# Performance work log

Measured on AMD Instinct MI355X. Metric: run time of the kernel, lower is better.

Reference implementation:

```python
import jax, jax.numpy as jnp
import numpy as np

N, E, D, ED = 50000, 800000, 64, 2


def setup_inputs() -> dict:
    key = jax.random.key(0)
    ks = jax.random.split(key, 16)
    inp = {
        "h": jax.random.normal(ks[0], (N, D), jnp.float32),
        "coord": jax.random.normal(ks[1], (N, 3), jnp.float32),
        "edge_index": jax.random.randint(ks[2], (2, E), 0, N, jnp.int32),
        "edge_attr": jax.random.normal(ks[3], (E, ED), jnp.float32),
        # edge_mlp: Linear(2D+1+ED -> D), Linear(D -> D)
        "W_e1": jax.random.normal(ks[4], (2 * D + 1 + ED, D), jnp.float32) * 0.08,
        "b_e1": jnp.zeros((D,), jnp.float32),
        "W_e2": jax.random.normal(ks[5], (D, D), jnp.float32) * 0.12,
        "b_e2": jnp.zeros((D,), jnp.float32),
        # node_mlp: Linear(D+D -> D), Linear(D -> D)
        "W_n1": jax.random.normal(ks[6], (2 * D, D), jnp.float32) * 0.08,
        "b_n1": jnp.zeros((D,), jnp.float32),
        "W_n2": jax.random.normal(ks[7], (D, D), jnp.float32) * 0.12,
        "b_n2": jnp.zeros((D,), jnp.float32),
        # coord_mlp: Linear(D -> D), Linear(D -> 1, bias=False, xavier gain 0.001)
        "W_c1": jax.random.normal(ks[8], (D, D), jnp.float32) * 0.12,
        "b_c1": jnp.zeros((D,), jnp.float32),
        "W_c2": jax.random.normal(ks[9], (D, 1), jnp.float32) * 1e-3,
    }
    return inp


def reference(h, coord, edge_index, edge_attr,
              W_e1, b_e1, W_e2, b_e2,
              W_n1, b_n1, W_n2, b_n2,
              W_c1, b_c1, W_c2):
    row, col = edge_index[0], edge_index[1]
    n_nodes = h.shape[0]

    # coord2radial
    coord_diff = coord[row] - coord[col]                       # [E,3]
    radial = jnp.sum(coord_diff * coord_diff, axis=-1, keepdims=True)  # [E,1]

    # edge_model
    e_in = jnp.concatenate([h[row], h[col], radial, edge_attr], axis=-1)  # [E, 2D+1+ED]
    e = jax.nn.silu(e_in @ W_e1 + b_e1)
    edge_feat = jax.nn.silu(e @ W_e2 + b_e2)                   # [E,D]

    # coord_model: trans = coord_diff * coord_mlp(edge_feat), clamp, segment mean
    scale = jax.nn.silu(edge_feat @ W_c1 + b_c1) @ W_c2        # [E,1]
    trans = jnp.clip(coord_diff * scale, -100.0, 100.0)        # [E,3]
    agg_c = jax.ops.segment_sum(trans, row, num_segments=n_nodes)       # [N,3]
    cnt = jax.ops.segment_sum(jnp.ones((trans.shape[0],), trans.dtype), row,
                              num_segments=n_nodes)            # [N]
    coord_out = coord + agg_c / jnp.clip(cnt, 1.0, None)[:, None]  # coords_weight=1.0

    # node_model: segment sum of edge_feat by row, node MLP, residual
    agg_h = jax.ops.segment_sum(edge_feat, row, num_segments=n_nodes)   # [N,D]
    n_in = jnp.concatenate([h, agg_h], axis=-1)                # [N,2D]
    h_out = h + (jax.nn.silu(n_in @ W_n1 + b_n1) @ W_n2 + b_n2)

    return (h_out, coord_out)
```

## Files before the change

kernel.cpp:

```cpp
#include <hip/hip_runtime.h>

#define DD 64
#define SLOTMAX 64

using s8v   = __attribute__((ext_vector_type(8))) short;
using f32x4 = __attribute__((ext_vector_type(4))) float;

typedef unsigned int   uint_t;
typedef unsigned short ushort_t;

union U8 { s8v v; uint_t u[4]; };

__device__ __forceinline__ float silu_f(float x) {
    return x / (1.0f + __expf(-x));
}
__device__ __forceinline__ float clamp100(float x) {
    return fminf(fmaxf(x, -100.0f), 100.0f);
}
__device__ __forceinline__ unsigned short f2bf(float x) {
    unsigned int u = __float_as_uint(x);
    return (unsigned short)((u + 0x7FFFu + ((u >> 16) & 1u)) >> 16);
}
__device__ __forceinline__ float bf2f(ushort_t v) {
    return __uint_as_float(((uint_t)v) << 16);
}
__device__ __forceinline__ uint_t cvt_pk_bf16(float lo, float hi) {
    uint_t r;
    asm("v_cvt_pk_bf16_f32 %0, %1, %2" : "=v"(r) : "v"(lo), "v"(hi));
    return r;
}

#define WAVE_FENCE() do { asm volatile("s_waitcnt lgkmcnt(0)" ::: "memory"); \
                          __builtin_amdgcn_sched_barrier(0); } while (0)

__global__ __launch_bounds__(256) void prep_all(
    const float* __restrict__ h,
    const float* __restrict__ coord,
    const float* __restrict__ We1, const float* __restrict__ We2,
    const float* __restrict__ Wc1,
    const float* __restrict__ Wn1, const float* __restrict__ Wn2,
    const float* __restrict__ be1, const float* __restrict__ be2,
    const float* __restrict__ bc1,
    const int*   __restrict__ ei,
    ushort_t* __restrict__ hbf,
    ushort_t* __restrict__ wf,
    float4* __restrict__ coord4,
    int* __restrict__ cnt_i,
    int N, int E, int total8, int histBlocks, int hbfBlocks, int c4Blocks)
{
    const int b = blockIdx.x;
    if (b < histBlocks) {
        const int e = b * 256 + threadIdx.x;
        if (e < E) atomicAdd(&cnt_i[ei[e]], 1);
    } else if (b < histBlocks + hbfBlocks) {
        const int t = (b - histBlocks) * 256 + threadIdx.x;
        if (t < total8) {
            const float4 v0 = ((const float4*)h)[t * 2 + 0];
            const float4 v1 = ((const float4*)h)[t * 2 + 1];
            uint4 o;
            o.x = (uint_t)f2bf(v0.x) | ((uint_t)f2bf(v0.y) << 16);
            o.y = (uint_t)f2bf(v0.z) | ((uint_t)f2bf(v0.w) << 16);
            o.z = (uint_t)f2bf(v1.x) | ((uint_t)f2bf(v1.y) << 16);
            o.w = (uint_t)f2bf(v1.z) | ((uint_t)f2bf(v1.w) << 16);
            ((uint4*)hbf)[t] = o;
        }
    } else if (b < histBlocks + hbfBlocks + c4Blocks) {
        const int t = (b - histBlocks - hbfBlocks) * 256 + threadIdx.x;
        if (t < N) {
            float4 c;
            c.x = coord[3 * t + 0];
            c.y = coord[3 * t + 1];
            c.z = coord[3 * t + 2];
            c.w = 0.0f;
            coord4[t] = c;
        }
    } else {
        const int t = (b - histBlocks - hbfBlocks - c4Blocks) * 256 + threadIdx.x;
        if (t >= 32768) return;
        if (t < 28672) {
            const int j    = t & 7;
            const int lane = (t >> 3) & 63;
            const int n0   = (t >> 9) & 3;
            const int k0   = (t >> 11) & 1;
            const int mat  = t >> 12;
            const int g    = lane >> 4;
            int k;
            if (mat == 2 || mat == 3) k = 16 * (2 * k0 + (j >> 2)) + 4 * g + (j & 3);
            else                      k = k0 * 32 + g * 8 + j;
            const int n = n0 * 16 + (lane & 15);
            float v;
            if      (mat == 0) v = We1[(size_t)k * 64 + n];
            else if (mat == 1) v = We1[(size_t)(64 + k) * 64 + n];
            else if (mat == 2) v = We2[(size_t)k * 64 + n];
            else if (mat == 3) v = Wc1[(size_t)k * 64 + n];
            else if (mat == 4) v = Wn1[(size_t)k * 64 + n];
            else if (mat == 5) v = Wn1[(size_t)(64 + k) * 64 + n];
            else               v = Wn2[(size_t)k * 64 + n];
            wf[t] = f2bf(v);
        } else {
            const int t2   = t - 28672;
            const int j    = t2 & 7;
            const int lane = (t2 >> 3) & 63;
            const int n0   = (t2 >> 9) & 3;
            const int xm   = (t2 >> 11) & 1;
            const int k = 8 * (lane >> 4) + j;
            const int m = n0 * 16 + (lane & 15);
            float v = 0.0f;
            if (xm == 0) {
                if      (k == 0) v = We1[(size_t)128 * 64 + m];
                else if (k == 1) v = We1[(size_t)129 * 64 + m];
                else if (k == 2) v = We1[(size_t)130 * 64 + m];
                else if (k == 3) v = be1[m];
            } else {
                if      (k == 0) v = be2[m];
                else if (k == 1) v = bc1[m];
            }
            wf[t] = f2bf(v);
        }
    }
}

__global__ __launch_bounds__(256) void prep_scan(
    const int* __restrict__ cnt_i,
    int* __restrict__ cursor,
    int* __restrict__ nstart,
    int N)
{
    __shared__ int sdata[256];
    __shared__ int sbase;
    const int tid = threadIdx.x;
    const int n = blockIdx.x * 256 + tid;
    int deg = 0;
    if (n < N) { deg = cnt_i[n]; if (deg > SLOTMAX) deg = SLOTMAX; }
    sdata[tid] = deg;
    __syncthreads();
    for (int off = 1; off < 256; off <<= 1) {
        const int t = (tid >= off) ? sdata[tid - off] : 0;
        __syncthreads();
        sdata[tid] += t;
        __syncthreads();
    }
    if (tid == 255) sbase = atomicAdd(cursor, sdata[255]);
    __syncthreads();
    if (n < N) nstart[n] = sbase + sdata[tid] - deg;
}

__global__ __launch_bounds__(256) void prep_fill(
    const int* __restrict__ ei,
    const float* __restrict__ ea,
    const int* __restrict__ nstart,
    int* __restrict__ cnt2,
    int4* __restrict__ eperm4,
    int E)
{
    const int e = blockIdx.x * 256 + threadIdx.x;
    if (e >= E) return;
    const int r = ei[e];
    const int s = atomicAdd(&cnt2[r], 1);
    if (s < SLOTMAX) {
        const int c = ei[E + e];
        const float2 a2 = *(const float2*)(ea + 2 * (size_t)e);
        const uint_t pk = cvt_pk_bf16(a2.x, a2.y);
        int4 v; v.x = r; v.y = c; v.z = (int)pk; v.w = 0;
        eperm4[(size_t)nstart[r] + s] = v;
    }
}

__global__ __launch_bounds__(512, 4) void egcl_edge(
    const ushort_t* __restrict__ hbf,
    const ushort_t* __restrict__ wfG,
    const float4* __restrict__ coord4,
    const int4* __restrict__ eperm4,
    const int* __restrict__ cursorP,
    const float* __restrict__ Wc2,
    uint_t* __restrict__ efu,
    float4* __restrict__ trans4,
    int totalWaves)
{
    __shared__ ushort_t fragLDS[20480];

    const int tid = threadIdx.x;
    #pragma unroll
    for (int i = 0; i < 4; ++i)
        ((uint4*)fragLDS)[tid + i * 512] = ((const uint4*)wfG)[tid + i * 512];
    ((uint4*)fragLDS)[2048 + tid] = ((const uint4*)wfG)[3584 + tid];
    __syncthreads();

    const int P = cursorP[0];
    const int wid  = tid >> 6;
    const int lane = tid & 63;
    const int l15  = lane & 15;
    const int g    = lane >> 4;

#define LD_W(mat, k0, m0) \
    (*(const s8v*)(fragLDS + ((((mat)*2 + (k0))*4 + (m0)) * 512) + lane * 8))
#define LD_X7(m0) (*(const s8v*)(fragLDS + 16384 + (m0) * 512 + lane * 8))
#define LD_XB(m0) (*(const s8v*)(fragLDS + 18432 + (m0) * 512 + lane * 8))

    float wc2_c[4][4];
    #pragma unroll
    for (int m0 = 0; m0 < 4; ++m0)
        #pragma unroll
        for (int j = 0; j < 4; ++j)
            wc2_c[m0][j] = Wc2[m0 * 16 + 4 * g + j];

    U8 b2f, bcf;
    b2f.u[0] = 0x00003F80u; b2f.u[1] = 0; b2f.u[2] = 0; b2f.u[3] = 0;
    bcf.u[0] = 0x3F800000u; bcf.u[1] = 0; bcf.u[2] = 0; bcf.u[3] = 0;

    const f32x4 zero4 = {0.f, 0.f, 0.f, 0.f};

    for (int t = blockIdx.x * 8 + wid; t * 16 < P; t += totalWaves) {
        const int p   = t * 16 + l15;
        const bool val = (p < P);
        const int pL  = val ? p : (P - 1);

        const int4 e4 = eperm4[pL];
        const int row = e4.x;
        const int col = e4.y;
        const uint_t eap = (uint_t)e4.z;

        const float4 cr = coord4[row];
        const float4 cc = coord4[col];
        const ushort_t* hr = hbf + (size_t)row * 64;
        const ushort_t* hc = hbf + (size_t)col * 64;
        const s8v br0 = *(const s8v*)(hr + g * 8);
        const s8v br1 = *(const s8v*)(hr + 32 + g * 8);
        const s8v bc0 = *(const s8v*)(hc + g * 8);
        const s8v bc1 = *(const s8v*)(hc + 32 + g * 8);

        const float dx = cr.x - cc.x, dy = cr.y - cc.y, dz = cr.z - cc.z;
        const float radial = dx * dx + dy * dy + dz * dz;

        U8 ex;
        const float ea0f = __uint_as_float(eap << 16);
        ex.u[0] = cvt_pk_bf16(radial, ea0f);
        ex.u[1] = (eap >> 16) | 0x3F800000u;
        ex.u[2] = 0; ex.u[3] = 0;

        f32x4 c1[4];
        #pragma unroll
        for (int m0 = 0; m0 < 4; ++m0) {
            f32x4 a = zero4;
            a = __builtin_amdgcn_mfma_f32_16x16x32_bf16(LD_W(0, 0, m0), br0, a, 0, 0, 0);
            a = __builtin_amdgcn_mfma_f32_16x16x32_bf16(LD_W(0, 1, m0), br1, a, 0, 0, 0);
            a = __builtin_amdgcn_mfma_f32_16x16x32_bf16(LD_W(1, 0, m0), bc0, a, 0, 0, 0);
            a = __builtin_amdgcn_mfma_f32_16x16x32_bf16(LD_W(1, 1, m0), bc1, a, 0, 0, 0);
            a = __builtin_amdgcn_mfma_f32_16x16x32_bf16(LD_X7(m0),      ex.v, a, 0, 0, 0);
            c1[m0] = a;
        }

        U8 f2a, f2b;
        #pragma unroll
        for (int m0 = 0; m0 < 4; ++m0) {
            const float ya = silu_f(c1[m0][0]);
            const float yb = silu_f(c1[m0][1]);
            const float yc = silu_f(c1[m0][2]);
            const float yd = silu_f(c1[m0][3]);
            U8& dst = (m0 < 2) ? f2a : f2b;
            dst.u[(m0 & 1) * 2 + 0] = cvt_pk_bf16(ya, yb);
            dst.u[(m0 & 1) * 2 + 1] = cvt_pk_bf16(yc, yd);
        }

        f32x4 c2[4];
        #pragma unroll
        for (int m0 = 0; m0 < 4; ++m0) {
            f32x4 a = zero4;
            a = __builtin_amdgcn_mfma_f32_16x16x32_bf16(LD_W(2, 0, m0), f2a.v, a, 0, 0, 0);
            a = __builtin_amdgcn_mfma_f32_16x16x32_bf16(LD_W(2, 1, m0), f2b.v, a, 0, 0, 0);
            a = __builtin_amdgcn_mfma_f32_16x16x32_bf16(LD_XB(m0),      b2f.v, a, 0, 0, 0);
            c2[m0] = a;
        }

        uint_t* efrow = efu + (size_t)pL * 32;
        U8 f3a, f3b;
        #pragma unroll
        for (int m0 = 0; m0 < 4; ++m0) {
            const float ya = silu_f(c2[m0][0]);
            const float yb = silu_f(c2[m0][1]);
            const float yc = silu_f(c2[m0][2]);
            const float yd = silu_f(c2[m0][3]);
            const uint_t p0 = cvt_pk_bf16(ya, yb);
            const uint_t p1 = cvt_pk_bf16(yc, yd);
            U8& dst = (m0 < 2) ? f3a : f3b;
            dst.u[(m0 & 1) * 2 + 0] = p0;
            dst.u[(m0 & 1) * 2 + 1] = p1;
            if (val) {
                uint2 st; st.x = p0; st.y = p1;
                *(uint2*)(efrow + m0 * 8 + g * 2) = st;
            }
        }

        float pacc = 0.f;
        #pragma unroll
        for (int m0 = 0; m0 < 4; ++m0) {
            f32x4 a = zero4;
            a = __builtin_amdgcn_mfma_f32_16x16x32_bf16(LD_W(3, 0, m0), f3a.v, a, 0, 0, 0);
            a = __builtin_amdgcn_mfma_f32_16x16x32_bf16(LD_W(3, 1, m0), f3b.v, a, 0, 0, 0);
            a = __builtin_amdgcn_mfma_f32_16x16x32_bf16(LD_XB(m0),      bcf.v, a, 0, 0, 0);
            #pragma unroll
            for (int j = 0; j < 4; ++j)
                pacc = fmaf(silu_f(a[j]), wc2_c[m0][j], pacc);
        }
        pacc += __shfl_xor(pacc, 16, 64);
        pacc += __shfl_xor(pacc, 32, 64);

        if (val && g == 0) {
            float4 tr;
            tr.x = clamp100(dx * pacc);
            tr.y = clamp100(dy * pacc);
            tr.z = clamp100(dz * pacc);
            tr.w = 0.0f;
            trans4[p] = tr;
        }
    }
#undef LD_W
#undef LD_X7
#undef LD_XB
}

__global__ __launch_bounds__(256) void egcl_agg(
    const ushort_t* __restrict__ efbf,
    const float4* __restrict__ trans4,
    const int* __restrict__ nstart,
    const int* __restrict__ cnt_i,
    const float4* __restrict__ coord4,
    ushort_t* __restrict__ aggbf,
    float* __restrict__ coord_out,
    int N)
{
    const int wid  = threadIdx.x >> 6;
    const int lane = threadIdx.x & 63;
    const int n = blockIdx.x * 4 + wid;
    if (n >= N) return;

    const int deg = cnt_i[n];
    const int eff = deg < SLOTMAX ? deg : SLOTMAX;
    const int p0  = nstart[n];

    const int sub = lane >> 4;
    const int dp  = lane & 15;

    float ax = 0.f, ay = 0.f, az = 0.f, aw = 0.f;
    for (int s = sub; s < eff; s += 4) {
        const uint2 v = *(const uint2*)(efbf + (size_t)(p0 + s) * 64 + dp * 4);
        ax += __uint_as_float(v.x << 16);
        ay += __uint_as_float(v.x & 0xFFFF0000u);
        az += __uint_as_float(v.y << 16);
        aw += __uint_as_float(v.y & 0xFFFF0000u);
    }
    ax += __shfl_xor(ax, 16, 64); ay += __shfl_xor(ay, 16, 64);
    az += __shfl_xor(az, 16, 64); aw += __shfl_xor(aw, 16, 64);
    ax += __shfl_xor(ax, 32, 64); ay += __shfl_xor(ay, 32, 64);
    az += __shfl_xor(az, 32, 64); aw += __shfl_xor(aw, 32, 64);
    if (sub == 0) {
        uint2 st;
        st.x = cvt_pk_bf16(ax, ay);
        st.y = cvt_pk_bf16(az, aw);
        *(uint2*)(aggbf + (size_t)n * 64 + dp * 4) = st;
    }

    float tx = 0.f, ty = 0.f, tz = 0.f;
    for (int s = lane; s < eff; s += 64) {
        const float4 tr = trans4[p0 + s];
        tx += tr.x; ty += tr.y; tz += tr.z;
    }
    #pragma unroll
    for (int msk = 1; msk < 64; msk <<= 1) {
        tx += __shfl_xor(tx, msk, 64);
        ty += __shfl_xor(ty, msk, 64);
        tz += __shfl_xor(tz, msk, 64);
    }
    if (lane == 0) {
        const float inv = 1.0f / fmaxf((float)deg, 1.0f);
        const float4 cn = coord4[n];
        coord_out[(size_t)n * 3 + 0] = cn.x + tx * inv;
        coord_out[(size_t)n * 3 + 1] = cn.y + ty * inv;
        coord_out[(size_t)n * 3 + 2] = cn.z + tz * inv;
    }
}

__global__ __launch_bounds__(512, 4) void egcl_node(
    const ushort_t* __restrict__ hbf,
    const ushort_t* __restrict__ aggbf,
    const ushort_t* __restrict__ wfG,
    const float* __restrict__ h,
    const float* __restrict__ bn1,
    const float* __restrict__ bn2,
    float* __restrict__ h_out,
    int N)
{
    __shared__ ushort_t fragLDS[12288];
    __shared__ ushort_t ldsY[8][16 * 72];

    const int tid = threadIdx.x;
    #pragma unroll
    for (int i = 0; i < 3; ++i)
        ((uint4*)fragLDS)[tid + i * 512] = ((const uint4*)(wfG + 16384))[tid + i * 512];
    __syncthreads();

    const int wid  = tid >> 6;
    const int lane = tid & 63;
    const int l15  = lane & 15;
    const int g    = lane >> 4;

#define LD_WN(mat, k0, n0) \
    (*(const s8v*)(fragLDS + ((((mat)*2 + (k0))*4 + (n0)) * 512) + lane * 8))

    float bn1_c[4], bn2_c[4];
    #pragma unroll
    for (int n0 = 0; n0 < 4; ++n0) {
        bn1_c[n0] = bn1[n0 * 16 + l15];
        bn2_c[n0] = bn2[n0 * 16 + l15];
    }

    const int wg = blockIdx.x * 8 + wid;
    const int nb = wg * 16;
    if (nb >= N) return;

    const int nod  = nb + l15;
    const int nodL = nod < N ? nod : N - 1;
    const ushort_t* hrow = hbf   + (size_t)nodL * 64;
    const ushort_t* arow = aggbf + (size_t)nodL * 64;
    const s8v aH0 = *(const s8v*)(hrow + g * 8);
    const s8v aH1 = *(const s8v*)(hrow + 32 + g * 8);
    const s8v aG0 = *(const s8v*)(arow + g * 8);
    const s8v aG1 = *(const s8v*)(arow + 32 + g * 8);

    ushort_t* yw = ldsY[wid];
    #pragma unroll
    for (int n0 = 0; n0 < 4; ++n0) {
        f32x4 a = {0.f, 0.f, 0.f, 0.f};
        a = __builtin_amdgcn_mfma_f32_16x16x32_bf16(aH0, LD_WN(0, 0, n0), a, 0, 0, 0);
        a = __builtin_amdgcn_mfma_f32_16x16x32_bf16(aH1, LD_WN(0, 1, n0), a, 0, 0, 0);
        a = __builtin_amdgcn_mfma_f32_16x16x32_bf16(aG0, LD_WN(1, 0, n0), a, 0, 0, 0);
        a = __builtin_amdgcn_mfma_f32_16x16x32_bf16(aG1, LD_WN(1, 1, n0), a, 0, 0, 0);
        #pragma unroll
        for (int jj = 0; jj < 4; ++jj)
            yw[(g * 4 + jj) * 72 + n0 * 16 + l15] = f2bf(silu_f(a[jj] + bn1_c[n0]));
    }
    WAVE_FENCE();

    const ushort_t* yrow = yw + l15 * 72;
    const s8v b0 = *(const s8v*)(yrow + g * 8);
    const s8v b1 = *(const s8v*)(yrow + 32 + g * 8);
    #pragma unroll
    for (int n0 = 0; n0 < 4; ++n0) {
        f32x4 a = {0.f, 0.f, 0.f, 0.f};
        a = __builtin_amdgcn_mfma_f32_16x16x32_bf16(b0, LD_WN(2, 0, n0), a, 0, 0, 0);
        a = __builtin_amdgcn_mfma_f32_16x16x32_bf16(b1, LD_WN(2, 1, n0), a, 0, 0, 0);
        #pragma unroll
        for (int jj = 0; jj < 4; ++jj) {
            const int m = nb + g * 4 + jj;
            if (m < N) {
                const size_t idx = (size_t)m * 64 + n0 * 16 + l15;
                h_out[idx] = h[idx] + (a[jj] + bn2_c[n0]);
            }
        }
    }
#undef LD_WN
}

extern "C" void kernel_launch(void* const* d_in, const int* in_sizes, int n_in,
                              void* d_out, int out_size, void* d_ws, size_t ws_size,
                              hipStream_t stream) {
    const float* h     = (const float*)d_in[0];
    const float* coord = (const float*)d_in[1];
    const int*   ei    = (const int*)  d_in[2];
    const float* ea    = (const float*)d_in[3];
    const float* We1   = (const float*)d_in[4];
    const float* be1   = (const float*)d_in[5];
    const float* We2   = (const float*)d_in[6];
    const float* be2   = (const float*)d_in[7];
    const float* Wn1   = (const float*)d_in[8];
    const float* bn1   = (const float*)d_in[9];
    const float* Wn2   = (const float*)d_in[10];
    const float* bn2   = (const float*)d_in[11];
    const float* Wc1   = (const float*)d_in[12];
    const float* bc1   = (const float*)d_in[13];
    const float* Wc2   = (const float*)d_in[14];

    const int N = in_sizes[0] / DD;
    const int E = in_sizes[3] / 2;

    float* out       = (float*)d_out;
    float* h_out     = out;
    float* coord_out = out + (size_t)N * DD;

    char* base = (char*)d_ws;
    ushort_t* hbf   = (ushort_t*)base;
    const size_t o_wf    = (size_t)N * DD * 2;
    ushort_t* wf    = (ushort_t*)(base + o_wf);
    const size_t o_agg   = o_wf + 32768 * 2;
    ushort_t* aggbf = (ushort_t*)(base + o_agg);
    const size_t o_c4    = o_agg + (size_t)N * DD * 2;
    float4* coord4  = (float4*)(base + o_c4);
    const size_t o_cnt   = o_c4 + (size_t)N * 16;
    int* cnt_i      = (int*)(base + o_cnt);
    int* cnt2       = cnt_i + N;
    int* cursor     = cnt_i + 2 * N;
    int* nstart     = cnt_i + 2 * N + 4;
    const size_t o_ep    = o_cnt + ((size_t)3 * N + 4) * 4 + 8;
    int4* eperm4    = (int4*)(base + ((o_ep + 15) & ~(size_t)15));
    const size_t o_tr    = ((o_ep + 15) & ~(size_t)15) + (size_t)E * 16;
    float4* trans4  = (float4*)(base + o_tr);
    const size_t o_ef    = o_tr + (size_t)E * 16;
    ushort_t* efbf  = (ushort_t*)(base + o_ef);

    hipMemsetAsync((void*)cnt_i, 0, ((size_t)2 * N + 4) * 4, stream);

    const int histBlocks = (E + 255) / 256;
    const int total8     = N * DD / 8;
    const int hbfBlocks  = (total8 + 255) / 256;
    const int c4Blocks   = (N + 255) / 256;
    const int wfBlocks   = (32768 + 255) / 256;
    prep_all<<<histBlocks + hbfBlocks + c4Blocks + wfBlocks, 256, 0, stream>>>(
        h, coord, We1, We2, Wc1, Wn1, Wn2, be1, be2, bc1, ei,
        hbf, wf, coord4, cnt_i, N, E, total8,
        histBlocks, hbfBlocks, c4Blocks);

    prep_scan<<<(N + 255) / 256, 256, 0, stream>>>(cnt_i, cursor, nstart, N);

    prep_fill<<<(E + 255) / 256, 256, 0, stream>>>(ei, ea, nstart, cnt2, eperm4, E);

    const int eblocks = 1024;
    const int totalWaves = eblocks * 8;
    egcl_edge<<<eblocks, 512, 0, stream>>>(
        hbf, wf, coord4, eperm4, cursor, Wc2,
        (uint_t*)efbf, trans4, totalWaves);

    const int ablocks = (N + 3) / 4;
    egcl_agg<<<ablocks, 256, 0, stream>>>(
        efbf, trans4, nstart, cnt_i, coord4, aggbf, coord_out, N);

    const int nwaves  = (N + 15) / 16;
    const int nblocks = (nwaves + 7) / 8;
    egcl_node<<<nblocks, 512, 0, stream>>>(
        hbf, aggbf, wf, h, bn1, bn2, h_out, N);
}
```

Before: 227.3 us.

## Fuse segment aggregation into edge kernel via in-wave segmented scan and atomics

The edge kernel no longer writes per-edge bf16 features and per-edge translations to global memory. It now runs a segmented prefix sum over each group of 16 row-sorted edges and atomically adds the partial sums into fp32 per-node accumulators. The separate aggregation kernel is removed, and the coordinate update moves into the node kernel, which now reads the fp32 aggregates and converts them to bf16. This removes large intermediate writes and re-reads plus one launch, at the cost of many shuffles, float atomics, an extra memset, and non-deterministic summation order.

```diff
diff --git a/kernel.cpp b/kernel.cpp
--- a/kernel.cpp
+++ b/kernel.cpp
@@ -20,9 +20,6 @@
 __device__ __forceinline__ unsigned short f2bf(float x) {
     unsigned int u = __float_as_uint(x);
     return (unsigned short)((u + 0x7FFFu + ((u >> 16) & 1u)) >> 16);
-}
-__device__ __forceinline__ float bf2f(ushort_t v) {
-    return __uint_as_float(((uint_t)v) << 16);
 }
 __device__ __forceinline__ uint_t cvt_pk_bf16(float lo, float hi) {
     uint_t r;
@@ -173,8 +170,8 @@
     const int4* __restrict__ eperm4,
     const int* __restrict__ cursorP,
     const float* __restrict__ Wc2,
-    uint_t* __restrict__ efu,
-    float4* __restrict__ trans4,
+    float* __restrict__ aggF,
+    float* __restrict__ transF,
     int totalWaves)
 {
     __shared__ ushort_t fragLDS[20480];
@@ -213,6 +210,7 @@
     for (int t = blockIdx.x * 8 + wid; t * 16 < P; t += totalWaves) {
         const int p   = t * 16 + l15;
         const bool val = (p < P);
+        const float valf = val ? 1.0f : 0.0f;
         const int pL  = val ? p : (P - 1);
 
         const int4 e4 = eperm4[pL];
@@ -272,7 +270,7 @@
             c2[m0] = a;
         }
 
-        uint_t* efrow = efu + (size_t)pL * 32;
+        float sef[4][4];
         U8 f3a, f3b;
         #pragma unroll
         for (int m0 = 0; m0 < 4; ++m0) {
@@ -280,15 +278,13 @@
             const float yb = silu_f(c2[m0][1]);
             const float yc = silu_f(c2[m0][2]);
             const float yd = silu_f(c2[m0][3]);
-            const uint_t p0 = cvt_pk_bf16(ya, yb);
-            const uint_t p1 = cvt_pk_bf16(yc, yd);
+            sef[m0][0] = ya * valf;
+            sef[m0][1] = yb * valf;
+            sef[m0][2] = yc * valf;
+            sef[m0][3] = yd * valf;
             U8& dst = (m0 < 2) ? f3a : f3b;
-            dst.u[(m0 & 1) * 2 + 0] = p0;
-            dst.u[(m0 & 1) * 2 + 1] = p1;
-            if (val) {
-                uint2 st; st.x = p0; st.y = p1;
-                *(uint2*)(efrow + m0 * 8 + g * 2) = st;
-            }
+            dst.u[(m0 & 1) * 2 + 0] = cvt_pk_bf16(ya, yb);
+            dst.u[(m0 & 1) * 2 + 1] = cvt_pk_bf16(yc, yd);
         }
 
         float pacc = 0.f;
@@ -305,13 +301,43 @@
         pacc += __shfl_xor(pacc, 16, 64);
         pacc += __shfl_xor(pacc, 32, 64);
 
-        if (val && g == 0) {
-            float4 tr;
-            tr.x = clamp100(dx * pacc);
-            tr.y = clamp100(dy * pacc);
-            tr.z = clamp100(dz * pacc);
-            tr.w = 0.0f;
-            trans4[p] = tr;
+        float tx = clamp100(dx * pacc) * valf;
+        float ty = clamp100(dy * pacc) * valf;
+        float tz = clamp100(dz * pacc) * valf;
+
+        const int rowN = __shfl_down(row, 1, 16);
+        const bool flush = (l15 == 15) || (rowN != row);
+
+        #pragma unroll
+        for (int d = 1; d < 16; d <<= 1) {
+            const int rup = __shfl_up(row, d, 16);
+            const float tk = ((l15 >= d) && (rup == row)) ? 1.0f : 0.0f;
+            #pragma unroll
+            for (int m0 = 0; m0 < 4; ++m0) {
+                #pragma unroll
+                for (int j = 0; j < 4; ++j) {
+                    const float u = __shfl_up(sef[m0][j], d, 16);
+                    sef[m0][j] = fmaf(u, tk, sef[m0][j]);
+                }
+            }
+            { const float u = __shfl_up(tx, d, 16); tx = fmaf(u, tk, tx); }
+            { const float u = __shfl_up(ty, d, 16); ty = fmaf(u, tk, ty); }
+            { const float u = __shfl_up(tz, d, 16); tz = fmaf(u, tk, tz); }
+        }
+
+        if (flush) {
+            float* ar = aggF + (size_t)row * 64 + 4 * g;
+            #pragma unroll
+            for (int m0 = 0; m0 < 4; ++m0) {
+                #pragma unroll
+                for (int j = 0; j < 4; ++j)
+                    atomicAdd(&ar[m0 * 16 + j], sef[m0][j]);
+            }
+            if (g == 0) {
+                atomicAdd(&transF[(size_t)row * 4 + 0], tx);
+                atomicAdd(&transF[(size_t)row * 4 + 1], ty);
+                atomicAdd(&transF[(size_t)row * 4 + 2], tz);
+            }
         }
     }
 #undef LD_W
@@ -319,75 +345,18 @@
 #undef LD_XB
 }
 
-__global__ __launch_bounds__(256) void egcl_agg(
-    const ushort_t* __restrict__ efbf,
-    const float4* __restrict__ trans4,
-    const int* __restrict__ nstart,
-    const int* __restrict__ cnt_i,
-    const float4* __restrict__ coord4,
-    ushort_t* __restrict__ aggbf,
-    float* __restrict__ coord_out,
-    int N)
-{
-    const int wid  = threadIdx.x >> 6;
-    const int lane = threadIdx.x & 63;
-    const int n = blockIdx.x * 4 + wid;
-    if (n >= N) return;
-
-    const int deg = cnt_i[n];
-    const int eff = deg < SLOTMAX ? deg : SLOTMAX;
-    const int p0  = nstart[n];
-
-    const int sub = lane >> 4;
-    const int dp  = lane & 15;
-
-    float ax = 0.f, ay = 0.f, az = 0.f, aw = 0.f;
-    for (int s = sub; s < eff; s += 4) {
-        const uint2 v = *(const uint2*)(efbf + (size_t)(p0 + s) * 64 + dp * 4);
-        ax += __uint_as_float(v.x << 16);
-        ay += __uint_as_float(v.x & 0xFFFF0000u);
-        az += __uint_as_float(v.y << 16);
-        aw += __uint_as_float(v.y & 0xFFFF0000u);
-    }
-    ax += __shfl_xor(ax, 16, 64); ay += __shfl_xor(ay, 16, 64);
-    az += __shfl_xor(az, 16, 64); aw += __shfl_xor(aw, 16, 64);
-    ax += __shfl_xor(ax, 32, 64); ay += __shfl_xor(ay, 32, 64);
-    az += __shfl_xor(az, 32, 64); aw += __shfl_xor(aw, 32, 64);
-    if (sub == 0) {
-        uint2 st;
-        st.x = cvt_pk_bf16(ax, ay);
-        st.y = cvt_pk_bf16(az, aw);
-        *(uint2*)(aggbf + (size_t)n * 64 + dp * 4) = st;
-    }
-
-    float tx = 0.f, ty = 0.f, tz = 0.f;
-    for (int s = lane; s < eff; s += 64) {
-        const float4 tr = trans4[p0 + s];
-        tx += tr.x; ty += tr.y; tz += tr.z;
-    }
-    #pragma unroll
-    for (int msk = 1; msk < 64; msk <<= 1) {
-        tx += __shfl_xor(tx, msk, 64);
-        ty += __shfl_xor(ty, msk, 64);
-        tz += __shfl_xor(tz, msk, 64);
-    }
-    if (lane == 0) {
-        const float inv = 1.0f / fmaxf((float)deg, 1.0f);
-        const float4 cn = coord4[n];
-        coord_out[(size_t)n * 3 + 0] = cn.x + tx * inv;
-        coord_out[(size_t)n * 3 + 1] = cn.y + ty * inv;
-        coord_out[(size_t)n * 3 + 2] = cn.z + tz * inv;
-    }
-}
-
 __global__ __launch_bounds__(512, 4) void egcl_node(
     const ushort_t* __restrict__ hbf,
-    const ushort_t* __restrict__ aggbf,
+    const float* __restrict__ aggF,
     const ushort_t* __restrict__ wfG,
     const float* __restrict__ h,
     const float* __restrict__ bn1,
     const float* __restrict__ bn2,
+    const float4* __restrict__ transF4,
+    const int* __restrict__ cnt_i,
+    const float4* __restrict__ coord4,
     float* __restrict__ h_out,
+    float* __restrict__ coord_out,
     int N)
 {
     __shared__ ushort_t fragLDS[12288];
@@ -420,21 +389,29 @@
 
     const int nod  = nb + l15;
     const int nodL = nod < N ? nod : N - 1;
-    const ushort_t* hrow = hbf   + (size_t)nodL * 64;
-    const ushort_t* arow = aggbf + (size_t)nodL * 64;
+    const ushort_t* hrow = hbf + (size_t)nodL * 64;
     const s8v aH0 = *(const s8v*)(hrow + g * 8);
     const s8v aH1 = *(const s8v*)(hrow + 32 + g * 8);
-    const s8v aG0 = *(const s8v*)(arow + g * 8);
-    const s8v aG1 = *(const s8v*)(arow + 32 + g * 8);
+
+    const float* arow = aggF + (size_t)nodL * 64;
+    const float4 va = *(const float4*)(arow + g * 8);
+    const float4 vb = *(const float4*)(arow + g * 8 + 4);
+    const float4 vc = *(const float4*)(arow + 32 + g * 8);
+    const float4 vd = *(const float4*)(arow + 32 + g * 8 + 4);
+    U8 g0, g1;
+    g0.u[0] = cvt_pk_bf16(va.x, va.y); g0.u[1] = cvt_pk_bf16(va.z, va.w);
+    g0.u[2] = cvt_pk_bf16(vb.x, vb.y); g0.u[3] = cvt_pk_bf16(vb.z, vb.w);
+    g1.u[0] = cvt_pk_bf16(vc.x, vc.y); g1.u[1] = cvt_pk_bf16(vc.z, vc.w);
+    g1.u[2] = cvt_pk_bf16(vd.x, vd.y); g1.u[3] = cvt_pk_bf16(vd.z, vd.w);
 
     ushort_t* yw = ldsY[wid];
     #pragma unroll
     for (int n0 = 0; n0 < 4; ++n0) {
         f32x4 a = {0.f, 0.f, 0.f, 0.f};
-        a = __builtin_amdgcn_mfma_f32_16x16x32_bf16(aH0, LD_WN(0, 0, n0), a, 0, 0, 0);
-        a = __builtin_amdgcn_mfma_f32_16x16x32_bf16(aH1, LD_WN(0, 1, n0), a, 0, 0, 0);
-        a = __builtin_amdgcn_mfma_f32_16x16x32_bf16(aG0, LD_WN(1, 0, n0), a, 0, 0, 0);
-        a = __builtin_amdgcn_mfma_f32_16x16x32_bf16(aG1, LD_WN(1, 1, n0), a, 0, 0, 0);
+        a = __builtin_amdgcn_mfma_f32_16x16x32_bf16(aH0,  LD_WN(0, 0, n0), a, 0, 0, 0);
+        a = __builtin_amdgcn_mfma_f32_16x16x32_bf16(aH1,  LD_WN(0, 1, n0), a, 0, 0, 0);
+        a = __builtin_amdgcn_mfma_f32_16x16x32_bf16(g0.v, LD_WN(1, 0, n0), a, 0, 0, 0);
+        a = __builtin_amdgcn_mfma_f32_16x16x32_bf16(g1.v, LD_WN(1, 1, n0), a, 0, 0, 0);
         #pragma unroll
         for (int jj = 0; jj < 4; ++jj)
             yw[(g * 4 + jj) * 72 + n0 * 16 + l15] = f2bf(silu_f(a[jj] + bn1_c[n0]));
@@ -457,6 +434,16 @@
                 h_out[idx] = h[idx] + (a[jj] + bn2_c[n0]);
             }
         }
+    }
+
+    if (g == 0 && nod < N) {
+        const float4 tf = transF4[nod];
+        const int dg = cnt_i[nod];
+        const float inv = 1.0f / fmaxf((float)dg, 1.0f);
+        const float4 cn = coord4[nod];
+        coord_out[(size_t)nod * 3 + 0] = cn.x + tf.x * inv;
+        coord_out[(size_t)nod * 3 + 1] = cn.y + tf.y * inv;
+        coord_out[(size_t)nod * 3 + 2] = cn.z + tf.z * inv;
     }
 #undef LD_WN
 }
@@ -491,23 +478,23 @@
     ushort_t* hbf   = (ushort_t*)base;
     const size_t o_wf    = (size_t)N * DD * 2;
     ushort_t* wf    = (ushort_t*)(base + o_wf);
-    const size_t o_agg   = o_wf + 32768 * 2;
-    ushort_t* aggbf = (ushort_t*)(base + o_agg);
-    const size_t o_c4    = o_agg + (size_t)N * DD * 2;
+    const size_t o_c4    = o_wf + 32768 * 2;
     float4* coord4  = (float4*)(base + o_c4);
     const size_t o_cnt   = o_c4 + (size_t)N * 16;
     int* cnt_i      = (int*)(base + o_cnt);
     int* cnt2       = cnt_i + N;
     int* cursor     = cnt_i + 2 * N;
     int* nstart     = cnt_i + 2 * N + 4;
-    const size_t o_ep    = o_cnt + ((size_t)3 * N + 4) * 4 + 8;
-    int4* eperm4    = (int4*)(base + ((o_ep + 15) & ~(size_t)15));
-    const size_t o_tr    = ((o_ep + 15) & ~(size_t)15) + (size_t)E * 16;
-    float4* trans4  = (float4*)(base + o_tr);
-    const size_t o_ef    = o_tr + (size_t)E * 16;
-    ushort_t* efbf  = (ushort_t*)(base + o_ef);
+    size_t o_ep = o_cnt + ((size_t)3 * N + 4) * 4;
+    o_ep = (o_ep + 15) & ~(size_t)15;
+    int4* eperm4    = (int4*)(base + o_ep);
+    const size_t o_agg   = o_ep + (size_t)E * 16;
+    float* aggF     = (float*)(base + o_agg);
+    const size_t o_tf    = o_agg + (size_t)N * DD * 4;
+    float* transF   = (float*)(base + o_tf);
 
     hipMemsetAsync((void*)cnt_i, 0, ((size_t)2 * N + 4) * 4, stream);
+    hipMemsetAsync((void*)aggF, 0, (size_t)N * DD * 4 + (size_t)N * 16, stream);
 
     const int histBlocks = (E + 255) / 256;
     const int total8     = N * DD / 8;
@@ -526,15 +513,11 @@
     const int eblocks = 1024;
     const int totalWaves = eblocks * 8;
     egcl_edge<<<eblocks, 512, 0, stream>>>(
-        hbf, wf, coord4, eperm4, cursor, Wc2,
-        (uint_t*)efbf, trans4, totalWaves);
-
-    const int ablocks = (N + 3) / 4;
-    egcl_agg<<<ablocks, 256, 0, stream>>>(
-        efbf, trans4, nstart, cnt_i, coord4, aggbf, coord_out, N);
+        hbf, wf, coord4, eperm4, cursor, Wc2, aggF, transF, totalWaves);
 
     const int nwaves  = (N + 15) / 16;
     const int nblocks = (nwaves + 7) / 8;
     egcl_node<<<nblocks, 512, 0, stream>>>(
-        hbf, aggbf, wf, h, bn1, bn2, h_out, N);
-}
+        hbf, aggF, wf, h, bn1, bn2,
+        (const float4*)transF, cnt_i, coord4, h_out, coord_out, N);
+}
```

After: 336.6 us. 1.48x slower.
